# Kernel tuning notes

Hardware: AMD Instinct MI355X
Metric: run time of the kernel (lower is better)

## Reference

```python
import jax, jax.numpy as jnp
import numpy as np

D_MODEL, N_HEADS, D_FF = 1024, 16, 4096
D_HEAD = D_MODEL // N_HEADS
B, S = 2, 2048
EPS = 1e-5


def setup_inputs() -> dict:
    key = jax.random.key(0)
    ks = jax.random.split(key, 12)
    sd = 1.0 / np.sqrt(D_MODEL)
    return {
        "x": jax.random.normal(ks[0], (B, S, D_MODEL), jnp.float32),
        "relative_bias": jax.random.normal(ks[1], (1, N_HEADS, S, S), jnp.float32),
        # attention projections, stored as (in, out) so y = x @ W
        "wq": jax.random.normal(ks[2], (D_MODEL, D_MODEL), jnp.float32) * sd,
        "wk": jax.random.normal(ks[3], (D_MODEL, D_MODEL), jnp.float32) * sd,
        "wv": jax.random.normal(ks[4], (D_MODEL, D_MODEL), jnp.float32) * sd,
        "wo": jax.random.normal(ks[5], (D_MODEL, D_MODEL), jnp.float32) * sd,
        "wo_b": jnp.zeros((D_MODEL,), jnp.float32),
        # FFN
        "w1": jax.random.normal(ks[6], (D_MODEL, D_FF), jnp.float32) * sd,
        "b1": jnp.zeros((D_FF,), jnp.float32),
        "w2": jax.random.normal(ks[7], (D_FF, D_MODEL), jnp.float32) * (1.0 / np.sqrt(D_FF)),
        "b2": jnp.zeros((D_MODEL,), jnp.float32),
        # LayerNorms
        "ln1_g": jnp.ones((D_MODEL,), jnp.float32),
        "ln1_b": jnp.zeros((D_MODEL,), jnp.float32),
        "ln2_g": jnp.ones((D_MODEL,), jnp.float32),
        "ln2_b": jnp.zeros((D_MODEL,), jnp.float32),
    }


def _layernorm(x, g, b):
    mu = jnp.mean(x, axis=-1, keepdims=True)
    var = jnp.mean(jnp.square(x - mu), axis=-1, keepdims=True)
    return (x - mu) * jax.lax.rsqrt(var + EPS) * g + b


def _attn(x, relative_bias, wq, wk, wv, wo, wo_b):
    b, s, d = x.shape
    # (B,S,D) -> (B,H,S,Dh)
    def split_heads(t):
        return t.reshape(b, s, N_HEADS, D_HEAD).transpose(0, 2, 1, 3)
    q = split_heads(x @ wq)
    k = split_heads(x @ wk)
    v = split_heads(x @ wv)
    scores = jnp.einsum("bhqd,bhkd->bhqk", q, k) / np.sqrt(D_HEAD) + relative_bias
    attn = jax.nn.softmax(scores, axis=-1)
    ctx = jnp.einsum("bhqk,bhkd->bhqd", attn, v)
    ctx = ctx.transpose(0, 2, 1, 3).reshape(b, s, d)
    return ctx @ wo + wo_b


def _ffn(x, w1, b1, w2, b2):
    return jax.nn.gelu(x @ w1 + b1, approximate=False) @ w2 + b2


def reference(x, relative_bias, wq, wk, wv, wo, wo_b, w1, b1, w2, b2,
              ln1_g, ln1_b, ln2_g, ln2_b):
    x = x + _attn(_layernorm(x, ln1_g, ln1_b), relative_bias, wq, wk, wv, wo, wo_b)
    x = x + _ffn(_layernorm(x, ln2_g, ln2_b), w1, b1, w2, b2)
    return x
```

## Files before the change

### kernel.cpp

```cpp
#include <hip/hip_runtime.h>
#include <hip/hip_bf16.h>
#include <stdint.h>

typedef unsigned short u16;
typedef __bf16 bf16x8 __attribute__((ext_vector_type(8)));
typedef u16   u16x8  __attribute__((ext_vector_type(8)));
typedef u16   u16x4  __attribute__((ext_vector_type(4)));
typedef u16   u16x2  __attribute__((ext_vector_type(2)));
typedef float f32x4  __attribute__((ext_vector_type(4)));

__device__ __forceinline__ u16 f2bf(float f) {
  union { float f; uint32_t u; } v; v.f = f;
  uint32_t r = v.u + 0x7fffu + ((v.u >> 16) & 1u);
  return (u16)(r >> 16);
}

typedef __attribute__((address_space(1))) void gvoid_t;
typedef __attribute__((address_space(3))) void lvoid_t;
__device__ __forceinline__ void gload_lds16(const void* g, void* l) {
  __builtin_amdgcn_global_load_lds((gvoid_t*)g, (lvoid_t*)l, 16, 0, 0);
}

template<int CTRL>
__device__ __forceinline__ float dpp_f(float x) {
  int i = __builtin_bit_cast(int, x);
  i = __builtin_amdgcn_update_dpp(i, i, CTRL, 0xF, 0xF, true);
  return __builtin_bit_cast(float, i);
}
__device__ __forceinline__ float rowmax16(float x) {
  x = fmaxf(x, dpp_f<0x128>(x));
  x = fmaxf(x, dpp_f<0x124>(x));
  x = fmaxf(x, dpp_f<0x122>(x));
  x = fmaxf(x, dpp_f<0x121>(x));
  return x;
}
__device__ __forceinline__ float rowsum16(float x) {
  x += dpp_f<0x128>(x);
  x += dpp_f<0x124>(x);
  x += dpp_f<0x122>(x);
  x += dpp_f<0x121>(x);
  return x;
}

__global__ __launch_bounds__(256)
void ln_kernel(const float* __restrict__ x, const float* __restrict__ g,
               const float* __restrict__ b, u16* __restrict__ out) {
  const int row = blockIdx.x;
  const int tid = threadIdx.x;
  const float* xr = x + (size_t)row * 1024;
  f32x4 v = *(const f32x4*)&xr[tid * 4];
  float s = v[0] + v[1] + v[2] + v[3];
  float q = v[0]*v[0] + v[1]*v[1] + v[2]*v[2] + v[3]*v[3];
  #pragma unroll
  for (int o = 32; o > 0; o >>= 1) { s += __shfl_xor(s, o); q += __shfl_xor(q, o); }
  __shared__ float ss[4], qq[4];
  if ((tid & 63) == 0) { ss[tid >> 6] = s; qq[tid >> 6] = q; }
  __syncthreads();
  s = ss[0] + ss[1] + ss[2] + ss[3];
  q = qq[0] + qq[1] + qq[2] + qq[3];
  float mu = s * (1.0f / 1024.0f);
  float var = q * (1.0f / 1024.0f) - mu * mu;
  float rstd = rsqrtf(var + 1e-5f);
  u16x4 o4;
  #pragma unroll
  for (int i = 0; i < 4; ++i)
    o4[i] = f2bf((v[i] - mu) * rstd * g[tid * 4 + i] + b[tid * 4 + i]);
  *(u16x4*)&out[(size_t)row * 1024 + tid * 4] = o4;
}

__global__ __launch_bounds__(256)
void transpose_cast(const float* __restrict__ W, u16* __restrict__ Wt, int K, int N) {
  __shared__ float t[32][33];
  const int n0 = blockIdx.x * 32, k0 = blockIdx.y * 32;
  const int tx = threadIdx.x & 31, ty = threadIdx.x >> 5;
  #pragma unroll
  for (int i = 0; i < 4; ++i)
    t[ty + 8*i][tx] = W[(size_t)(k0 + ty + 8*i) * N + n0 + tx];
  __syncthreads();
  #pragma unroll
  for (int i = 0; i < 4; ++i)
    Wt[(size_t)(n0 + ty + 8*i) * K + k0 + tx] = f2bf(t[tx][ty + 8*i]);
}

template<int EPI>
__global__ __launch_bounds__(256, 2)
void gemm_bt(const u16* __restrict__ A, const u16* __restrict__ Bt,
             void* __restrict__ out, const float* __restrict__ bias,
             const float* __restrict__ resid, int M, int N, int K) {
  __shared__ u16 As[128 * 32];
  __shared__ u16 Bs[128 * 32];
  const int tid = threadIdx.x;
  const int w = tid >> 6, l = tid & 63;
  const int bm = blockIdx.x * 128, bn = blockIdx.y * 128;
  const int wr = (w >> 1) * 64, wc = (w & 1) * 64;
  const int l15 = l & 15, lhi = l >> 4;
  f32x4 acc[4][4] = {};

  const int r4 = tid >> 2;
  const int c8 = (tid & 3) * 8;
  const u16* ga0 = A  + (size_t)(bm + r4) * K + c8;
  const u16* ga1 = ga0 + (size_t)64 * K;
  const u16* gb0 = Bt + (size_t)(bn + r4) * K + c8;
  const u16* gb1 = gb0 + (size_t)64 * K;
  u16* lA0 = &As[(w * 16) * 32];
  u16* lA1 = &As[(64 + w * 16) * 32];
  u16* lB0 = &Bs[(w * 16) * 32];
  u16* lB1 = &Bs[(64 + w * 16) * 32];

  const int arow = (wr + l15) * 32 + lhi * 8;
  const int brow = (wc + l15) * 32 + lhi * 8;

  for (int k0 = 0; k0 < K; k0 += 32) {
    gload_lds16(ga0 + k0, lA0);
    gload_lds16(ga1 + k0, lA1);
    gload_lds16(gb0 + k0, lB0);
    gload_lds16(gb1 + k0, lB1);
    __syncthreads();
    bf16x8 a[4], b[4];
    #pragma unroll
    for (int m = 0; m < 4; ++m) a[m] = *(const bf16x8*)&As[arow + m * 16 * 32];
    #pragma unroll
    for (int n = 0; n < 4; ++n) b[n] = *(const bf16x8*)&Bs[brow + n * 16 * 32];
    #pragma unroll
    for (int m = 0; m < 4; ++m)
      #pragma unroll
      for (int n = 0; n < 4; ++n)
        acc[m][n] = __builtin_amdgcn_mfma_f32_16x16x32_bf16(a[m], b[n], acc[m][n], 0, 0, 0);
    __syncthreads();
  }

  #pragma unroll
  for (int m = 0; m < 4; ++m) {
    #pragma unroll
    for (int n = 0; n < 4; ++n) {
      #pragma unroll
      for (int r = 0; r < 4; ++r) {
        const int grow = bm + wr + m * 16 + lhi * 4 + r;
        const int gcol = bn + wc + n * 16 + l15;
        float vv = acc[m][n][r];
        if constexpr (EPI >= 1) vv += bias[gcol];
        if constexpr (EPI == 1) vv = 0.5f * vv * (1.0f + erff(vv * 0.70710678118f));
        if constexpr (EPI == 2) {
          vv += resid[(size_t)grow * N + gcol];
          ((float*)out)[(size_t)grow * N + gcol] = vv;
        } else {
          ((u16*)out)[(size_t)grow * N + gcol] = f2bf(vv);
        }
      }
    }
  }
}

#define SWZ(row) ((((row) & 7) ^ (((row) >> 3) & 7)) << 3)

__global__ __launch_bounds__(256)
void attn_kernel(const u16* __restrict__ qkv, const float* __restrict__ bias,
                 u16* __restrict__ ctx) {
  const int qt = blockIdx.x;
  const int bh = blockIdx.y;
  const int b = bh >> 4, h = bh & 15;
  const int tid = threadIdx.x, w = tid >> 6, l = tid & 63;
  const int l15 = l & 15, lhi = l >> 4;
  const size_t ld = 3072;
  const float L2E = 1.44269504f;

  __shared__ u16 Kl[2][4096];
  __shared__ u16 Vt[2][4096];
  __shared__ u16 Pl[4][1024];

  const u16* qp = qkv;
  const u16* kp = qkv + 1024;
  const u16* vp = qkv + 2048;

  const int key2 = (tid >> 3) * 2, dg8 = (tid & 7) * 8;
  const u16* kbase = kp + ((size_t)b * 2048 + key2) * ld + h * 64 + dg8;
  const u16* vbase = vp + ((size_t)b * 2048 + key2) * ld + h * 64 + dg8;

  bf16x8 qf0, qf1;
  {
    const u16* qrow = qp + ((size_t)b * 2048 + qt * 64 + w * 16 + l15) * ld + h * 64 + lhi * 8;
    qf0 = *(const bf16x8*)qrow;
    qf1 = *(const bf16x8*)(qrow + 32);
  }

  const float* bg0 = bias + ((size_t)h * 2048 + qt * 64 + w * 16 + lhi * 4) * 2048 + l15;
  const float* bp0 = bg0;
  const float* bp1 = bg0 + 2048;
  const float* bp2 = bg0 + 4096;
  const float* bp3 = bg0 + 6144;

  float m_run[4], s_run[4];
  f32x4 octx[4] = {};
  #pragma unroll
  for (int r = 0; r < 4; ++r) { m_run[r] = -1e30f; s_run[r] = 0.f; }

  u16x8 kpf[2], vpf[2];
  float bf[16];

  auto load_kv = [&](int kv) {
    kpf[0] = *(const u16x8*)(kbase + (size_t)kv * ld);
    kpf[1] = *(const u16x8*)(kbase + (size_t)(kv + 1) * ld);
    vpf[0] = *(const u16x8*)(vbase + (size_t)kv * ld);
    vpf[1] = *(const u16x8*)(vbase + (size_t)(kv + 1) * ld);
  };
  auto load_bias = [&]() {
    bf[0]  = bp0[0];  bf[1]  = bp0[16]; bf[2]  = bp0[32]; bf[3]  = bp0[48];
    bf[4]  = bp1[0];  bf[5]  = bp1[16]; bf[6]  = bp1[32]; bf[7]  = bp1[48];
    bf[8]  = bp2[0];  bf[9]  = bp2[16]; bf[10] = bp2[32]; bf[11] = bp2[48];
    bf[12] = bp3[0];  bf[13] = bp3[16]; bf[14] = bp3[32]; bf[15] = bp3[48];
    bp0 += 64; bp1 += 64; bp2 += 64; bp3 += 64;
  };
  auto store_kv = [&](u16* Kd, u16* Vd) {
    *(u16x8*)&Kd[(key2)     * 64 + (dg8 ^ SWZ(key2))]     = kpf[0];
    *(u16x8*)&Kd[(key2 + 1) * 64 + (dg8 ^ SWZ(key2 + 1))] = kpf[1];
    #pragma unroll
    for (int i = 0; i < 8; ++i) {
      const int d = dg8 + i;
      u16x2 vq = { vpf[0][i], vpf[1][i] };
      *(u16x2*)&Vd[d * 64 + (key2 ^ SWZ(d))] = vq;
    }
  };

  load_kv(0);
  load_bias();
  store_kv(Kl[0], Vt[0]);
  load_kv(64);
  __syncthreads();

  for (int it = 0; it < 32; ++it) {
    const int cur = it & 1, nxt = cur ^ 1;
    if (it < 31) store_kv(Kl[nxt], Vt[nxt]);
    if (it < 30) load_kv((it + 2) * 64);

    f32x4 sa[4] = {};
    #pragma unroll
    for (int nf = 0; nf < 4; ++nf) {
      const int row = nf * 16 + l15;
      const int s = SWZ(row);
      bf16x8 kf0 = *(const bf16x8*)&Kl[cur][row * 64 + ((lhi * 8) ^ s)];
      bf16x8 kf1 = *(const bf16x8*)&Kl[cur][row * 64 + ((32 + lhi * 8) ^ s)];
      sa[nf] = __builtin_amdgcn_mfma_f32_16x16x32_bf16(qf0, kf0, sa[nf], 0, 0, 0);
      sa[nf] = __builtin_amdgcn_mfma_f32_16x16x32_bf16(qf1, kf1, sa[nf], 0, 0, 0);
    }

    float p[4][4];
    #pragma unroll
    for (int r = 0; r < 4; ++r)
      #pragma unroll
      for (int nf = 0; nf < 4; ++nf)
        p[r][nf] = fmaf(sa[nf][r], 0.125f, bf[r * 4 + nf]);
    if (it < 31) load_bias();

    #pragma unroll
    for (int r = 0; r < 4; ++r) {
      float mx = fmaxf(fmaxf(p[r][0], p[r][1]), fmaxf(p[r][2], p[r][3]));
      mx = rowmax16(mx);
      if (mx > m_run[r] + 5.545177f) {
        const float fs = exp2f((m_run[r] - mx) * L2E);
        s_run[r] *= fs;
        #pragma unroll
        for (int nf = 0; nf < 4; ++nf) octx[nf][r] *= fs;
        m_run[r] = mx;
      }
      const float nml = -m_run[r] * L2E;
      float e0 = exp2f(fmaf(p[r][0], L2E, nml));
      float e1 = exp2f(fmaf(p[r][1], L2E, nml));
      float e2 = exp2f(fmaf(p[r][2], L2E, nml));
      float e3 = exp2f(fmaf(p[r][3], L2E, nml));
      p[r][0] = e0; p[r][1] = e1; p[r][2] = e2; p[r][3] = e3;
      s_run[r] += rowsum16((e0 + e1) + (e2 + e3));
    }

    #pragma unroll
    for (int r = 0; r < 4; ++r) {
      const int row = lhi * 4 + r;
      const int s = SWZ(row);
      #pragma unroll
      for (int nf = 0; nf < 4; ++nf)
        Pl[w][row * 64 + ((nf * 16 + l15) ^ s)] =
            __builtin_bit_cast(u16, (__bf16)p[r][nf]);
    }

    #pragma unroll
    for (int ks = 0; ks < 2; ++ks) {
      bf16x8 pa = *(const bf16x8*)&Pl[w][l15 * 64 + ((ks * 32 + lhi * 8) ^ SWZ(l15))];
      #pragma unroll
      for (int nf = 0; nf < 4; ++nf) {
        const int row = nf * 16 + l15;
        bf16x8 bv = *(const bf16x8*)&Vt[cur][row * 64 + ((ks * 32 + lhi * 8) ^ SWZ(row))];
        octx[nf] = __builtin_amdgcn_mfma_f32_16x16x32_bf16(pa, bv, octx[nf], 0, 0, 0);
      }
    }

    __syncthreads();
  }

  float inv[4];
  #pragma unroll
  for (int r = 0; r < 4; ++r) inv[r] = 1.0f / s_run[r];
  #pragma unroll
  for (int nf = 0; nf < 4; ++nf)
    #pragma unroll
    for (int r = 0; r < 4; ++r) {
      const int grow = b * 2048 + qt * 64 + w * 16 + lhi * 4 + r;
      const int gcol = h * 64 + nf * 16 + l15;
      ctx[(size_t)grow * 1024 + gcol] = f2bf(octx[nf][r] * inv[r]);
    }
}

extern "C" void kernel_launch(void* const* d_in, const int* in_sizes, int n_in,
                              void* d_out, int out_size, void* d_ws, size_t ws_size,
                              hipStream_t stream) {
  const float* x    = (const float*)d_in[0];
  const float* rb   = (const float*)d_in[1];
  const float* wq   = (const float*)d_in[2];
  const float* wk   = (const float*)d_in[3];
  const float* wv   = (const float*)d_in[4];
  const float* wo   = (const float*)d_in[5];
  const float* wo_b = (const float*)d_in[6];
  const float* w1   = (const float*)d_in[7];
  const float* b1   = (const float*)d_in[8];
  const float* w2   = (const float*)d_in[9];
  const float* b2   = (const float*)d_in[10];
  const float* ln1g = (const float*)d_in[11];
  const float* ln1b = (const float*)d_in[12];
  const float* ln2g = (const float*)d_in[13];
  const float* ln2b = (const float*)d_in[14];

  char* ws = (char*)d_ws;
  u16*   xn    = (u16*)(ws + 0);
  u16*   qkvb  = (u16*)(ws + (8u << 20));
  u16*   hbuf  = (u16*)(ws + (8u << 20));
  u16*   ctxb  = (u16*)(ws + (32u << 20));
  float* x1    = (float*)(ws + (40u << 20));
  u16*   wqkvt = (u16*)(ws + (56u << 20));
  u16*   wot   = (u16*)(ws + (62u << 20));
  u16*   w1t   = (u16*)(ws + (64u << 20));
  u16*   w2t   = (u16*)(ws + (72u << 20));

  transpose_cast<<<dim3(32, 32),  256, 0, stream>>>(wq, wqkvt,               1024, 1024);
  transpose_cast<<<dim3(32, 32),  256, 0, stream>>>(wk, wqkvt + 1024 * 1024, 1024, 1024);
  transpose_cast<<<dim3(32, 32),  256, 0, stream>>>(wv, wqkvt + 2048 * 1024, 1024, 1024);
  transpose_cast<<<dim3(32, 32),  256, 0, stream>>>(wo, wot,                 1024, 1024);
  transpose_cast<<<dim3(128, 32), 256, 0, stream>>>(w1, w1t,                 1024, 4096);
  transpose_cast<<<dim3(32, 128), 256, 0, stream>>>(w2, w2t,                 4096, 1024);

  ln_kernel<<<4096, 256, 0, stream>>>(x, ln1g, ln1b, xn);
  gemm_bt<0><<<dim3(32, 24), 256, 0, stream>>>(xn, wqkvt, qkvb, nullptr, nullptr, 4096, 3072, 1024);
  attn_kernel<<<dim3(32, 32), 256, 0, stream>>>(qkvb, rb, ctxb);
  gemm_bt<2><<<dim3(32, 8), 256, 0, stream>>>(ctxb, wot, x1, wo_b, x, 4096, 1024, 1024);
  ln_kernel<<<4096, 256, 0, stream>>>(x1, ln2g, ln2b, xn);
  gemm_bt<1><<<dim3(32, 32), 256, 0, stream>>>(xn, w1t, hbuf, b1, nullptr, 4096, 4096, 1024);
  gemm_bt<2><<<dim3(32, 8), 256, 0, stream>>>(hbuf, w2t, (float*)d_out, b2, x1, 4096, 1024, 4096);

  (void)in_sizes; (void)n_in; (void)out_size; (void)ws_size;
}
```

Before: 399.5 us.

## Double-buffer attention bias loads and add 64-row GEMM for N=1024 projections

The attention loop now keeps two register buffers of relative-bias values and unrolls by two, so each bias tile is fetched a full iteration earlier, hiding global-load latency behind more compute. Separately, a new 64x128-tile GEMM with two blocks per CU replaces the 128-row tiles for the output projection and the FFN down-projection, doubling the grid from 256 to 512 blocks to fill more CUs. The added bias registers raise register pressure in the attention kernel. The smaller GEMM tiles lower data reuse per block, and the new kernel is single-buffered.

```diff
diff --git a/kernel.cpp b/kernel.cpp
--- a/kernel.cpp
+++ b/kernel.cpp
@@ -151,6 +151,72 @@
   }
 }
 
+template<int EPI>
+__global__ __launch_bounds__(256, 2)
+void gemm_bt64(const u16* __restrict__ A, const u16* __restrict__ Bt,
+               void* __restrict__ out, const float* __restrict__ bias,
+               const float* __restrict__ resid, int M, int N, int K) {
+  __shared__ u16 As[64 * 32];
+  __shared__ u16 Bs[128 * 32];
+  const int tid = threadIdx.x;
+  const int w = tid >> 6, l = tid & 63;
+  const int bm = blockIdx.x * 64, bn = blockIdx.y * 128;
+  const int wr = (w & 1) * 32, wc = (w >> 1) * 64;
+  const int l15 = l & 15, lhi = l >> 4;
+  f32x4 acc[2][4] = {};
+
+  const int r4 = tid >> 2;
+  const int c8 = (tid & 3) * 8;
+  const u16* ga0 = A  + (size_t)(bm + r4) * K + c8;
+  const u16* gb0 = Bt + (size_t)(bn + r4) * K + c8;
+  const u16* gb1 = gb0 + (size_t)64 * K;
+  u16* lA0 = &As[(w * 16) * 32];
+  u16* lB0 = &Bs[(w * 16) * 32];
+  u16* lB1 = &Bs[(64 + w * 16) * 32];
+
+  const int arow = (wr + l15) * 32 + lhi * 8;
+  const int brow = (wc + l15) * 32 + lhi * 8;
+
+  for (int k0 = 0; k0 < K; k0 += 32) {
+    gload_lds16(ga0 + k0, lA0);
+    gload_lds16(gb0 + k0, lB0);
+    gload_lds16(gb1 + k0, lB1);
+    __syncthreads();
+    bf16x8 a[2], b[4];
+    #pragma unroll
+    for (int m = 0; m < 2; ++m) a[m] = *(const bf16x8*)&As[arow + m * 16 * 32];
+    #pragma unroll
+    for (int n = 0; n < 4; ++n) b[n] = *(const bf16x8*)&Bs[brow + n * 16 * 32];
+    #pragma unroll
+    for (int m = 0; m < 2; ++m)
+      #pragma unroll
+      for (int n = 0; n < 4; ++n)
+        acc[m][n] = __builtin_amdgcn_mfma_f32_16x16x32_bf16(a[m], b[n], acc[m][n], 0, 0, 0);
+    __syncthreads();
+  }
+
+  #pragma unroll
+  for (int m = 0; m < 2; ++m) {
+    #pragma unroll
+    for (int n = 0; n < 4; ++n) {
+      #pragma unroll
+      for (int r = 0; r < 4; ++r) {
+        const int grow = bm + wr + m * 16 + lhi * 4 + r;
+        const int gcol = bn + wc + n * 16 + l15;
+        float vv = acc[m][n][r];
+        if constexpr (EPI >= 1) vv += bias[gcol];
+        if constexpr (EPI == 1) vv = 0.5f * vv * (1.0f + erff(vv * 0.70710678118f));
+        if constexpr (EPI == 2) {
+          vv += resid[(size_t)grow * N + gcol];
+          ((float*)out)[(size_t)grow * N + gcol] = vv;
+        } else {
+          ((u16*)out)[(size_t)grow * N + gcol] = f2bf(vv);
+        }
+      }
+    }
+  }
+}
+
 #define SWZ(row) ((((row) & 7) ^ (((row) >> 3) & 7)) << 3)
 
 __global__ __launch_bounds__(256)
@@ -195,7 +261,7 @@
   for (int r = 0; r < 4; ++r) { m_run[r] = -1e30f; s_run[r] = 0.f; }
 
   u16x8 kpf[2], vpf[2];
-  float bf[16];
+  float bfA[16], bfB[16];
 
   auto load_kv = [&](int kv) {
     kpf[0] = *(const u16x8*)(kbase + (size_t)kv * ld);
@@ -203,7 +269,7 @@
     vpf[0] = *(const u16x8*)(vbase + (size_t)kv * ld);
     vpf[1] = *(const u16x8*)(vbase + (size_t)(kv + 1) * ld);
   };
-  auto load_bias = [&]() {
+  auto load_bias = [&](float (&bf)[16]) {
     bf[0]  = bp0[0];  bf[1]  = bp0[16]; bf[2]  = bp0[32]; bf[3]  = bp0[48];
     bf[4]  = bp1[0];  bf[5]  = bp1[16]; bf[6]  = bp1[32]; bf[7]  = bp1[48];
     bf[8]  = bp2[0];  bf[9]  = bp2[16]; bf[10] = bp2[32]; bf[11] = bp2[48];
@@ -222,14 +288,14 @@
   };
 
   load_kv(0);
-  load_bias();
+  load_bias(bfA);
+  load_bias(bfB);
   store_kv(Kl[0], Vt[0]);
   load_kv(64);
   __syncthreads();
 
-  for (int it = 0; it < 32; ++it) {
-    const int cur = it & 1, nxt = cur ^ 1;
-    if (it < 31) store_kv(Kl[nxt], Vt[nxt]);
+  auto iter = [&](int it, int cur, float (&bc)[16]) {
+    if (it < 31) store_kv(Kl[cur ^ 1], Vt[cur ^ 1]);
     if (it < 30) load_kv((it + 2) * 64);
 
     f32x4 sa[4] = {};
@@ -248,8 +314,8 @@
     for (int r = 0; r < 4; ++r)
       #pragma unroll
       for (int nf = 0; nf < 4; ++nf)
-        p[r][nf] = fmaf(sa[nf][r], 0.125f, bf[r * 4 + nf]);
-    if (it < 31) load_bias();
+        p[r][nf] = fmaf(sa[nf][r], 0.125f, bc[r * 4 + nf]);
+    if (it < 30) load_bias(bc);
 
     #pragma unroll
     for (int r = 0; r < 4; ++r) {
@@ -293,6 +359,11 @@
     }
 
     __syncthreads();
+  };
+
+  for (int i2 = 0; i2 < 16; ++i2) {
+    iter(2 * i2,     0, bfA);
+    iter(2 * i2 + 1, 1, bfB);
   }
 
   float inv[4];
@@ -348,10 +419,10 @@
   ln_kernel<<<4096, 256, 0, stream>>>(x, ln1g, ln1b, xn);
   gemm_bt<0><<<dim3(32, 24), 256, 0, stream>>>(xn, wqkvt, qkvb, nullptr, nullptr, 4096, 3072, 1024);
   attn_kernel<<<dim3(32, 32), 256, 0, stream>>>(qkvb, rb, ctxb);
-  gemm_bt<2><<<dim3(32, 8), 256, 0, stream>>>(ctxb, wot, x1, wo_b, x, 4096, 1024, 1024);
+  gemm_bt64<2><<<dim3(64, 8), 256, 0, stream>>>(ctxb, wot, x1, wo_b, x, 4096, 1024, 1024);
   ln_kernel<<<4096, 256, 0, stream>>>(x1, ln2g, ln2b, xn);
   gemm_bt<1><<<dim3(32, 32), 256, 0, stream>>>(xn, w1t, hbuf, b1, nullptr, 4096, 4096, 1024);
-  gemm_bt<2><<<dim3(32, 8), 256, 0, stream>>>(hbuf, w2t, (float*)d_out, b2, x1, 4096, 1024, 4096);
+  gemm_bt64<2><<<dim3(64, 8), 256, 0, stream>>>(hbuf, w2t, (float*)d_out, b2, x1, 4096, 1024, 4096);
 
   (void)in_sizes; (void)n_in; (void)out_size; (void)ws_size;
 }
```

Result: no change. 404.8 us (+1.3%).
